# Optimization experiments

Measured on AMD Instinct MI355X. Metric: run time of the kernel, lower is better.

## Reference

```python
import jax, jax.numpy as jnp
import numpy as np

B, S, DIN, DH = 8, 8192, 256, 256


def setup_inputs() -> dict:
    key = jax.random.key(0)
    k0, k1, k2, k3, k4 = jax.random.split(key, 5)
    stdv = 1.0 / np.sqrt(DIN)
    x = jax.random.normal(k0, (B, S, DIN), jnp.float32)
    W0 = jax.random.uniform(k1, (2 * DH, DIN), jnp.float32, -stdv, stdv)
    b0 = jax.random.uniform(k2, (2 * DH,), jnp.float32, -stdv, stdv)
    stdv2 = 1.0 / np.sqrt(DH)
    W1 = jax.random.uniform(k3, (2 * DH, DH), jnp.float32, -stdv2, stdv2)
    b1 = jax.random.uniform(k4, (2 * DH,), jnp.float32, -stdv2, stdv2)
    return {"x": x, "W0": W0, "b0": b0, "W1": W1, "b1": b1}


def _log_g(x):
    # log of g(x) = x + 0.5 for x >= 0 else sigmoid(x)
    return jnp.where(x >= 0, jnp.log(jax.nn.relu(x) + 0.5), -jax.nn.softplus(-x))


def _mingru_layer(x, W, b):
    # x: (B,S,Din); W: (2*DH, Din); b: (2*DH,)
    gh = jnp.einsum('bsd,ed->bse', x, W) + b          # (B,S,2*DH)
    gate, hidden = jnp.split(gh, 2, axis=-1)          # each (B,S,DH)
    log_coeffs = -jax.nn.softplus(gate)               # log(1 - z)
    log_vals = -jax.nn.softplus(-gate) + _log_g(hidden)  # log z + log h_tilde
    Bb, Ss, Dd = log_coeffs.shape
    # initial hidden h0 = g(0) = 0.5  ->  log(h0) = log(0.5)
    log_h0 = jnp.full((Bb, 1, Dd), jnp.log(0.5), log_coeffs.dtype)
    log_values = jnp.concatenate([log_h0, log_vals], axis=1)          # (B,S+1,DH)
    a_star = jnp.concatenate(
        [jnp.zeros((Bb, 1, Dd), log_coeffs.dtype), jnp.cumsum(log_coeffs, axis=1)],
        axis=1)                                                       # (B,S+1,DH)
    log_h = a_star + jax.lax.cumlogsumexp(log_values - a_star, axis=1)
    return jnp.exp(log_h)[:, 1:]                                      # (B,S,DH)


def reference(x, W0, b0, W1, b1):
    out0 = _mingru_layer(x, W0, b0)
    out1 = _mingru_layer(out0, W1, b1)
    h = jnp.stack([out0[:, -1:], out1[:, -1:]])  # (num_layers,B,1,DH)
    return out1, h
```

## Files before the change

### kernel.cpp

```cpp
#include <hip/hip_runtime.h>
#include <hip/hip_bf16.h>

#define Bb 8
#define Ss 8192
#define Dd 256
#define Mm (Bb * Ss)
#define Nn 512
#define NCHUNK 128
#define CLEN (Ss / NCHUNK)

typedef __hip_bfloat16 bf16;
typedef __attribute__((ext_vector_type(8))) short short8;
typedef __attribute__((ext_vector_type(4))) float f32x4;

__device__ __forceinline__ void load_lds16(const void* g, void* l) {
  __builtin_amdgcn_global_load_lds(
      (const __attribute__((address_space(1))) void*)g,
      (__attribute__((address_space(3))) void*)l, 16, 0, 0);
}

__global__ __launch_bounds__(256) void cvt_f32_bf16(const float* __restrict__ in,
                                                    bf16* __restrict__ out,
                                                    long n4) {
  long i = (long)blockIdx.x * blockDim.x + threadIdx.x;
  if (i >= n4) return;
  const float4 v = ((const float4*)in)[i];
  union { ushort4 u; bf16 h[4]; } o;
  o.h[0] = __float2bfloat16(v.x);
  o.h[1] = __float2bfloat16(v.y);
  o.h[2] = __float2bfloat16(v.z);
  o.h[3] = __float2bfloat16(v.w);
  ((ushort4*)out)[i] = o.u;
}

__device__ __forceinline__ void av_from_gh(float gate, float hid, float& a,
                                           float& v) {
  gate = fminf(fmaxf(gate, -20.f), 20.f);
  float eg = __expf(gate);
  a = 1.f / (1.f + eg);
  float z = eg * a;
  float gfun;
  if (hid >= 0.f) {
    gfun = hid + 0.5f;
  } else {
    float eh = __expf(fmaxf(hid, -20.f));
    gfun = eh / (1.f + eh);
  }
  v = z * gfun;
}

__device__ __forceinline__ unsigned pack_av(float a, float v) {
  union { bf16 h[2]; unsigned u; } o;
  o.h[0] = __float2bfloat16(a);
  o.h[1] = __float2bfloat16(v);
  return o.u;
}

template <bool F32A>
__global__ __launch_bounds__(256) void gemm_av_fused(
    const void* __restrict__ Xv, const bf16* __restrict__ W,
    const float* __restrict__ bias, unsigned* __restrict__ AV,
    float* __restrict__ Asum, float* __restrict__ Vsum) {
  constexpr int ABY = F32A ? 16384 : 8192;
  __shared__ __align__(16) char sm[2 * ABY + 16384];
  char* Abuf0 = sm;
  char* Abuf1 = sm + ABY;
  bf16* Bbuf0 = (bf16*)(sm + 2 * ABY);
  bf16* Bbuf1 = (bf16*)(sm + 2 * ABY + 8192);
  unsigned* Ts = (unsigned*)sm;

  const int tid = threadIdx.x;
  const int w = tid >> 6;
  const int l = tid & 63;
  const int fl = l & 15;
  const int q = l >> 4;

  const int cb = blockIdx.x;
  const int bt = blockIdx.y;
  const long rowBase = (long)bt * 128;
  const int wrow = (w >> 1) * 64;
  const int wc = (w & 1) * 32;

  const float* Xf = (const float*)Xv;
  const bf16* Xb = (const bf16*)Xv;

  auto stageA = [&](char* dst, int k0) {
    if constexpr (F32A) {
#pragma unroll
      for (int c = 0; c < 4; c++) {
        const int L = c * 256 + tid;
        const int row = L >> 3;
        const int kc = (L & 7) ^ (row & 7);
        load_lds16(Xf + (rowBase + row) * 256 + k0 + kc * 4,
                   dst + (c * 256 + w * 64) * 16);
      }
    } else {
#pragma unroll
      for (int c = 0; c < 2; c++) {
        const int L = c * 256 + tid;
        const int row = L >> 2;
        const int kc = (L & 3) ^ ((row >> 1) & 3);
        load_lds16(Xb + (rowBase + row) * 256 + k0 + kc * 8,
                   dst + (c * 256 + w * 64) * 16);
      }
    }
  };
  auto stageB = [&](bf16* dst, int k0) {
#pragma unroll
    for (int c = 0; c < 2; c++) {
      const int L = c * 256 + tid;
      const int row = L >> 2;
      const int kc = (L & 3) ^ ((row >> 1) & 3);
      const int grow = (row < 64) ? (cb * 64 + row) : (192 + cb * 64 + row);
      load_lds16(W + (long)grow * 256 + k0 + kc * 8,
                 (char*)dst + (c * 256 + w * 64) * 16);
    }
  };

  auto fragA = [&](const char* buf, int mt) -> short8 {
    const int row = wrow + 16 * mt + fl;
    if constexpr (F32A) {
      const float* p = (const float*)buf + row * 32;
      const int k0c = (2 * q) ^ (row & 7);
      const int k1c = (2 * q + 1) ^ (row & 7);
      const float4 u0 = *(const float4*)(p + k0c * 4);
      const float4 u1 = *(const float4*)(p + k1c * 4);
      const float vals[8] = {u0.x, u0.y, u0.z, u0.w, u1.x, u1.y, u1.z, u1.w};
      short8 r;
#pragma unroll
      for (int i = 0; i < 8; i++) {
        union { bf16 h; short s; } t;
        t.h = __float2bfloat16(vals[i]);
        r[i] = t.s;
      }
      return r;
    } else {
      const int kc = q ^ ((row >> 1) & 3);
      return *(const short8*)((const bf16*)buf + row * 32 + kc * 8);
    }
  };
  auto fragB = [&](const bf16* buf, int nt) -> short8 {
    const int row =
        (nt < 2) ? (wc + 16 * nt + fl) : (64 + wc + 16 * (nt - 2) + fl);
    const int kc = q ^ ((row >> 1) & 3);
    return *(const short8*)(buf + row * 32 + kc * 8);
  };

  f32x4 acc[4][4];
#pragma unroll
  for (int i = 0; i < 4; i++)
#pragma unroll
    for (int j = 0; j < 4; j++) acc[i][j] = (f32x4)0.0f;

  stageA(Abuf0, 0);
  stageB(Bbuf0, 0);
  __syncthreads();
#pragma unroll
  for (int ks = 0; ks < 8; ks++) {
    const char* Ac = (ks & 1) ? Abuf1 : Abuf0;
    const bf16* Bc = (ks & 1) ? Bbuf1 : Bbuf0;
    if (ks < 7) {
      stageA((ks & 1) ? Abuf0 : Abuf1, (ks + 1) * 32);
      stageB((ks & 1) ? Bbuf0 : Bbuf1, (ks + 1) * 32);
    }
    short8 af[4], bf_[4];
#pragma unroll
    for (int mt = 0; mt < 4; mt++) af[mt] = fragA(Ac, mt);
#pragma unroll
    for (int nt = 0; nt < 4; nt++) bf_[nt] = fragB(Bc, nt);
#pragma unroll
    for (int mt = 0; mt < 4; mt++)
#pragma unroll
      for (int nt = 0; nt < 4; nt++)
        acc[mt][nt] = __builtin_amdgcn_mfma_f32_16x16x32_bf16(
            af[mt], bf_[nt], acc[mt][nt], 0, 0, 0);
    __syncthreads();
  }

  float bg[2], bh[2];
#pragma unroll
  for (int p = 0; p < 2; p++) {
    const int d = cb * 64 + wc + 16 * p + fl;
    bg[p] = bias[d];
    bh[p] = bias[256 + d];
  }
  unsigned pk[4][2][4];
#pragma unroll
  for (int mt = 0; mt < 4; mt++) {
#pragma unroll
    for (int p = 0; p < 2; p++) {
      const int d = cb * 64 + wc + 16 * p + fl;
      const long r0 = rowBase + wrow + 16 * mt + q * 4;
#pragma unroll
      for (int r = 0; r < 4; r++) {
        float a, v;
        av_from_gh(acc[mt][p][r] + bg[p], acc[mt][p + 2][r] + bh[p], a, v);
        pk[mt][p][r] = pack_av(a, v);
        AV[(r0 + r) * 256 + d] = pk[mt][p][r];
      }
    }
  }

#pragma unroll
  for (int h = 0; h < 2; h++) {
    if ((w >> 1) == h) {
#pragma unroll
      for (int mt = 0; mt < 4; mt++)
#pragma unroll
        for (int p = 0; p < 2; p++)
#pragma unroll
          for (int r = 0; r < 4; r++)
            Ts[(16 * mt + 4 * q + r) * 65 + wc + 16 * p + fl] = pk[mt][p][r];
    }
    __syncthreads();
    if (tid < 64) {
      float A = 1.f, H = 0.f;
#pragma unroll 8
      for (int t = 0; t < 64; t++) {
        const unsigned p = Ts[t * 65 + tid];
        const float a = __uint_as_float((p & 0xffffu) << 16);
        const float v = __uint_as_float(p & 0xffff0000u);
        A *= a;
        H = a * H + v;
      }
      const long cg = (long)(bt >> 6) * NCHUNK + ((bt & 63) << 1) + h;
      Asum[cg * 256 + cb * 64 + tid] = A;
      Vsum[cg * 256 + cb * 64 + tid] = H;
    }
    __syncthreads();
  }
}

__global__ __launch_bounds__(256) void scan_combine(
    const float* __restrict__ Asum, const float* __restrict__ Vsum,
    float* __restrict__ Hin) {
  const int d = threadIdx.x;
  const int b = blockIdx.x;
  float h = 0.5f;
#pragma unroll 8
  for (int c = 0; c < NCHUNK; c++) {
    const long i = ((long)b * NCHUNK + c) * 256 + d;
    Hin[i] = h;
    h = Asum[i] * h + Vsum[i];
  }
}

template <bool WRITE_BF16>
__global__ __launch_bounds__(256) void scan_final(
    const unsigned* __restrict__ AV, const float* __restrict__ Hin,
    bf16* __restrict__ OutB, float* __restrict__ OutF,
    float* __restrict__ Hlast) {
  const int d = threadIdx.x;
  const int c = blockIdx.x % NCHUNK;
  const int b = blockIdx.x / NCHUNK;
  float h = Hin[(long)blockIdx.x * 256 + d];
  long base = ((long)b * Ss + (long)c * CLEN) * 256 + d;
#pragma unroll 8
  for (int t = 0; t < CLEN; t++) {
    const unsigned p = AV[base];
    const float a = __uint_as_float((p & 0xffffu) << 16);
    const float v = __uint_as_float(p & 0xffff0000u);
    h = a * h + v;
    if (WRITE_BF16)
      OutB[base] = __float2bfloat16(h);
    else
      OutF[base] = h;
    base += 256;
  }
  if (c == NCHUNK - 1) Hlast[b * 256 + d] = h;
}

extern "C" void kernel_launch(void* const* d_in, const int* in_sizes, int n_in,
                              void* d_out, int out_size, void* d_ws,
                              size_t ws_size, hipStream_t stream) {
  const float* x = (const float*)d_in[0];
  const float* W0f = (const float*)d_in[1];
  const float* b0 = (const float*)d_in[2];
  const float* W1f = (const float*)d_in[3];
  const float* b1 = (const float*)d_in[4];

  float* outF = (float*)d_out;
  float* hlast = outF + (long)Mm * 256;
  bf16* Xb = (bf16*)d_out;

  char* ws = (char*)d_ws;
  unsigned* AV = (unsigned*)ws;
  bf16* W0b = (bf16*)(ws + (long)Mm * 256 * 4);
  bf16* W1b = W0b + (long)Nn * Dd;
  float* Asum = (float*)(W1b + (long)Nn * Dd);
  float* Vsum = Asum + (long)Bb * NCHUNK * 256;
  float* Hin = Vsum + (long)Bb * NCHUNK * 256;

  const dim3 gemmGrid(4, Mm / 128);
  const dim3 blk(256);
  const dim3 scanGrid(Bb * NCHUNK);

  {
    const long n4w = (long)Nn * Dd / 4;
    cvt_f32_bf16<<<dim3((n4w + 255) / 256), blk, 0, stream>>>(W0f, W0b, n4w);
    cvt_f32_bf16<<<dim3((n4w + 255) / 256), blk, 0, stream>>>(W1f, W1b, n4w);
  }

  gemm_av_fused<true><<<gemmGrid, blk, 0, stream>>>(x, W0b, b0, AV, Asum,
                                                    Vsum);
  scan_combine<<<dim3(Bb), blk, 0, stream>>>(Asum, Vsum, Hin);
  scan_final<true><<<scanGrid, blk, 0, stream>>>(AV, Hin, Xb, nullptr, hlast);

  gemm_av_fused<false><<<gemmGrid, blk, 0, stream>>>(Xb, W1b, b1, AV, Asum,
                                                     Vsum);
  scan_combine<<<dim3(Bb), blk, 0, stream>>>(Asum, Vsum, Hin);
  scan_final<false><<<scanGrid, blk, 0, stream>>>(AV, Hin, nullptr, outF,
                                                  hlast + Bb * 256);
}
```

Baseline: 269.8 us.

## Prefetch two K-stages ahead with vmcnt waits and remap GEMM block order

The GEMM main loop now issues the first two K-stages up front. Each iteration waits on vmcnt so only the current stage's global-to-LDS loads must finish, which keeps one stage of loads in flight during the MFMA work instead of a full __syncthreads drain. Buffers are refilled two stages ahead after a barrier. The grid also becomes 1D with a swizzled block-to-tile mapping that spreads neighbouring blocks across XCDs/rows, aiming for better L2 reuse. The code depends on the hand-counted vmcnt values (6 or 4 loads per stage) being correct.

```diff
diff --git a/kernel.cpp b/kernel.cpp
--- a/kernel.cpp
+++ b/kernel.cpp
@@ -17,6 +17,18 @@
   __builtin_amdgcn_global_load_lds(
       (const __attribute__((address_space(1))) void*)g,
       (__attribute__((address_space(3))) void*)l, 16, 0, 0);
+}
+
+template <int N>
+__device__ __forceinline__ void wait_vmcnt() {
+  if constexpr (N == 0)
+    asm volatile("s_waitcnt vmcnt(0)" ::: "memory");
+  else if constexpr (N == 4)
+    asm volatile("s_waitcnt vmcnt(4)" ::: "memory");
+  else if constexpr (N == 6)
+    asm volatile("s_waitcnt vmcnt(6)" ::: "memory");
+  else
+    static_assert(N == 0 || N == 4 || N == 6, "unsupported vmcnt");
 }
 
 __global__ __launch_bounds__(256) void cvt_f32_bf16(const float* __restrict__ in,
@@ -62,6 +74,7 @@
     const float* __restrict__ bias, unsigned* __restrict__ AV,
     float* __restrict__ Asum, float* __restrict__ Vsum) {
   constexpr int ABY = F32A ? 16384 : 8192;
+  constexpr int NLD = F32A ? 6 : 4;
   __shared__ __align__(16) char sm[2 * ABY + 16384];
   char* Abuf0 = sm;
   char* Abuf1 = sm + ABY;
@@ -75,8 +88,10 @@
   const int fl = l & 15;
   const int q = l >> 4;
 
-  const int cb = blockIdx.x;
-  const int bt = blockIdx.y;
+  const int id = blockIdx.x;
+  const int lin = ((id & 7) << 8) | (id >> 3);
+  const int cb = lin & 3;
+  const int bt = lin >> 2;
   const long rowBase = (long)bt * 128;
   const int wrow = (w >> 1) * 64;
   const int wc = (w & 1) * 32;
@@ -154,15 +169,18 @@
 
   stageA(Abuf0, 0);
   stageB(Bbuf0, 0);
-  __syncthreads();
+  stageA(Abuf1, 32);
+  stageB(Bbuf1, 32);
 #pragma unroll
   for (int ks = 0; ks < 8; ks++) {
-    const char* Ac = (ks & 1) ? Abuf1 : Abuf0;
-    const bf16* Bc = (ks & 1) ? Bbuf1 : Bbuf0;
-    if (ks < 7) {
-      stageA((ks & 1) ? Abuf0 : Abuf1, (ks + 1) * 32);
-      stageB((ks & 1) ? Bbuf0 : Bbuf1, (ks + 1) * 32);
-    }
+    char* Ac = (ks & 1) ? Abuf1 : Abuf0;
+    bf16* Bc = (ks & 1) ? Bbuf1 : Bbuf0;
+    if (ks < 7)
+      wait_vmcnt<NLD>();
+    else
+      wait_vmcnt<0>();
+    __builtin_amdgcn_s_barrier();
+    __builtin_amdgcn_sched_barrier(0);
     short8 af[4], bf_[4];
 #pragma unroll
     for (int mt = 0; mt < 4; mt++) af[mt] = fragA(Ac, mt);
@@ -174,7 +192,12 @@
       for (int nt = 0; nt < 4; nt++)
         acc[mt][nt] = __builtin_amdgcn_mfma_f32_16x16x32_bf16(
             af[mt], bf_[nt], acc[mt][nt], 0, 0, 0);
-    __syncthreads();
+    asm volatile("s_waitcnt lgkmcnt(0)" ::: "memory");
+    __builtin_amdgcn_s_barrier();
+    if (ks < 6) {
+      stageA(Ac, (ks + 2) * 32);
+      stageB(Bc, (ks + 2) * 32);
+    }
   }
 
   float bg[2], bh[2];
@@ -291,7 +314,7 @@
   float* Vsum = Asum + (long)Bb * NCHUNK * 256;
   float* Hin = Vsum + (long)Bb * NCHUNK * 256;
 
-  const dim3 gemmGrid(4, Mm / 128);
+  const dim3 gemmGrid(2048);
   const dim3 blk(256);
   const dim3 scanGrid(Bb * NCHUNK);
 
```

Result: no change. 267.0 us (-1.0%).
